# Optimization experiments

Measured on AMD Instinct MI355X. Metric: run time of the kernel, lower is better.

The kernel has to match this reference:

```python
import jax, jax.numpy as jnp
import numpy as np

TEMPERATURE = 32.0  # sqrt(d_model=1024)

def setup_inputs() -> dict:
    key = jax.random.key(0)
    kq, kk, kv = jax.random.split(key, 3)
    B, H, S, D = 2, 16, 2048, 64
    q = jax.random.normal(kq, (B, H, S, D), dtype=jnp.float32)
    k = jax.random.normal(kk, (B, H, S, D), dtype=jnp.float32)
    v = jax.random.normal(kv, (B, H, S, D), dtype=jnp.float32)
    mask = jnp.ones((B, 1, 1, S), dtype=jnp.int32)  # key-padding mask, 1 = keep
    return {"q": q, "k": k, "v": v, "mask": mask}

def reference(q, k, v, mask):
    # scores: [B,H,S,S]
    scores = jnp.einsum('bhqd,bhkd->bhqk', q / TEMPERATURE, k)
    scores = jnp.where(mask == 0, jnp.float32(-1e9), scores)
    attention = jax.nn.softmax(scores, axis=-1)
    # dropout is identity at inference (module's nn.Dropout in eval mode)
    output = jnp.einsum('bhqk,bhkd->bhqd', attention, v)
    return (output, attention)
```

## Files before the change

kernel.cpp:

```cpp
#include <hip/hip_runtime.h>
#include <hip/hip_bf16.h>


#define S_LEN 2048
#define D_DIM 64
#define BM 64
#define BN 64
#define NT (S_LEN / BN)
#define LDP 72

typedef __attribute__((ext_vector_type(8))) short bf16x8;
typedef __attribute__((ext_vector_type(4))) float f32x4;

__device__ __forceinline__ unsigned short f2bf(float x) {
    unsigned u = __float_as_uint(x);
    u += 0x7FFF + ((u >> 16) & 1);
    return (unsigned short)(u >> 16);
}

__global__ __launch_bounds__(256, 4)
void attn_kernel(const float* __restrict__ Qg, const float* __restrict__ Kg,
                 const float* __restrict__ Vg, const int* __restrict__ Mg,
                 float* __restrict__ Og, float* __restrict__ Ag) {
    __shared__ unsigned short Qs[BM * LDP];
    __shared__ unsigned short Ks[BN * LDP];
    __shared__ unsigned short Vts[D_DIM * LDP];
    __shared__ unsigned short Ps[BM * LDP];
    __shared__ int maskS[BN];

    const int tid  = threadIdx.x;
    const int w    = tid >> 6;
    const int lane = tid & 63;
    const int l15  = lane & 15;
    const int quad = lane >> 4;

    const int qt = blockIdx.x;
    const int bh = blockIdx.y;
    const int b  = bh >> 4;
    const int q0 = qt * BM;

    const float* Qb = Qg + ((size_t)bh * S_LEN + q0) * D_DIM;
    const float* Kb = Kg + (size_t)bh * S_LEN * D_DIM;
    const float* Vb = Vg + (size_t)bh * S_LEN * D_DIM;
    const int*   Mb = Mg + (size_t)b * S_LEN;
    float* Ob = Og + ((size_t)bh * S_LEN + q0) * D_DIM;
    float* Ab = Ag + ((size_t)bh * S_LEN + q0) * (size_t)S_LEN;

    {
        const float sc = 1.0f / 32.0f;
        #pragma unroll
        for (int i = 0; i < 4; ++i) {
            int f = tid + i * 256;
            int row = f >> 4, c4 = f & 15;
            const float4 v = *(const float4*)(Qb + row * D_DIM + c4 * 4);
            unsigned lo = f2bf(v.x * sc) | ((unsigned)f2bf(v.y * sc) << 16);
            unsigned hi = f2bf(v.z * sc) | ((unsigned)f2bf(v.w * sc) << 16);
            *(uint2*)(&Qs[row * LDP + c4 * 4]) = make_uint2(lo, hi);
        }
    }
    __syncthreads();

    bf16x8 aq[2];
    #pragma unroll
    for (int ks = 0; ks < 2; ++ks)
        aq[ks] = *(const bf16x8*)(&Qs[(w * 16 + l15) * LDP + ks * 32 + quad * 8]);

    float lsum[4] = {0.f, 0.f, 0.f, 0.f};

    for (int kt = 0; kt < NT; ++kt) {
        const int key0 = kt * BN;
        #pragma unroll
        for (int i = 0; i < 4; ++i) {
            int f = tid + i * 256;
            int row = f >> 4, c4 = f & 15;
            const float4 v = *(const float4*)(Kb + (size_t)(key0 + row) * D_DIM + c4 * 4);
            unsigned lo = f2bf(v.x) | ((unsigned)f2bf(v.y) << 16);
            unsigned hi = f2bf(v.z) | ((unsigned)f2bf(v.w) << 16);
            *(uint2*)(&Ks[row * LDP + c4 * 4]) = make_uint2(lo, hi);
        }
        if (tid < BN) maskS[tid] = Mb[key0 + tid];
        __syncthreads();

        #pragma unroll
        for (int cb = 0; cb < 4; ++cb) {
            f32x4 acc = {0.f, 0.f, 0.f, 0.f};
            #pragma unroll
            for (int ks = 0; ks < 2; ++ks) {
                bf16x8 bk = *(const bf16x8*)(&Ks[(cb * 16 + l15) * LDP + ks * 32 + quad * 8]);
                acc = __builtin_amdgcn_mfma_f32_16x16x32_bf16(aq[ks], bk, acc, 0, 0, 0);
            }
            const int mk = maskS[cb * 16 + l15];
            #pragma unroll
            for (int r = 0; r < 4; ++r) {
                float s = mk ? acc[r] : -1e9f;
                lsum[r] += __expf(s);
            }
        }
        __syncthreads();
    }

    #pragma unroll
    for (int r = 0; r < 4; ++r) {
        float v = lsum[r];
        v += __shfl_xor(v, 1);
        v += __shfl_xor(v, 2);
        v += __shfl_xor(v, 4);
        v += __shfl_xor(v, 8);
        lsum[r] = 1.0f / v;
    }

    f32x4 oacc[4];
    #pragma unroll
    for (int db = 0; db < 4; ++db) oacc[db] = (f32x4){0.f, 0.f, 0.f, 0.f};

    for (int kt = 0; kt < NT; ++kt) {
        const int key0 = kt * BN;
        #pragma unroll
        for (int i = 0; i < 4; ++i) {
            int f = tid + i * 256;
            int row = f >> 4, c4 = f & 15;
            const float4 v = *(const float4*)(Kb + (size_t)(key0 + row) * D_DIM + c4 * 4);
            unsigned lo = f2bf(v.x) | ((unsigned)f2bf(v.y) << 16);
            unsigned hi = f2bf(v.z) | ((unsigned)f2bf(v.w) << 16);
            *(uint2*)(&Ks[row * LDP + c4 * 4]) = make_uint2(lo, hi);
        }
        {
            int key = tid & 63, g = tid >> 6;
            #pragma unroll
            for (int i = 0; i < 4; ++i) {
                int d0 = (g * 4 + i) * 4;
                const float4 v = *(const float4*)(Vb + (size_t)(key0 + key) * D_DIM + d0);
                Vts[(d0 + 0) * LDP + key] = f2bf(v.x);
                Vts[(d0 + 1) * LDP + key] = f2bf(v.y);
                Vts[(d0 + 2) * LDP + key] = f2bf(v.z);
                Vts[(d0 + 3) * LDP + key] = f2bf(v.w);
            }
        }
        if (tid < BN) maskS[tid] = Mb[key0 + tid];
        __syncthreads();

        #pragma unroll
        for (int cb = 0; cb < 4; ++cb) {
            f32x4 acc = {0.f, 0.f, 0.f, 0.f};
            #pragma unroll
            for (int ks = 0; ks < 2; ++ks) {
                bf16x8 bk = *(const bf16x8*)(&Ks[(cb * 16 + l15) * LDP + ks * 32 + quad * 8]);
                acc = __builtin_amdgcn_mfma_f32_16x16x32_bf16(aq[ks], bk, acc, 0, 0, 0);
            }
            const int mk  = maskS[cb * 16 + l15];
            const int key = key0 + cb * 16 + l15;
            #pragma unroll
            for (int r = 0; r < 4; ++r) {
                float s = mk ? acc[r] : -1e9f;
                float p = __expf(s) * lsum[r];
                int row = w * 16 + quad * 4 + r;
                Ab[(size_t)row * S_LEN + key] = p;
                Ps[row * LDP + cb * 16 + l15] = f2bf(p);
            }
        }
        #pragma unroll
        for (int ks2 = 0; ks2 < 2; ++ks2) {
            bf16x8 ap = *(const bf16x8*)(&Ps[(w * 16 + l15) * LDP + ks2 * 32 + quad * 8]);
            #pragma unroll
            for (int db = 0; db < 4; ++db) {
                bf16x8 bv = *(const bf16x8*)(&Vts[(db * 16 + l15) * LDP + ks2 * 32 + quad * 8]);
                oacc[db] = __builtin_amdgcn_mfma_f32_16x16x32_bf16(ap, bv, oacc[db], 0, 0, 0);
            }
        }
        __syncthreads();
    }

    #pragma unroll
    for (int db = 0; db < 4; ++db) {
        #pragma unroll
        for (int r = 0; r < 4; ++r) {
            int row = w * 16 + quad * 4 + r;
            Ob[(size_t)row * D_DIM + db * 16 + l15] = oacc[db][r];
        }
    }
}

extern "C" void kernel_launch(void* const* d_in, const int* in_sizes, int n_in,
                              void* d_out, int out_size, void* d_ws, size_t ws_size,
                              hipStream_t stream) {
    const float* q = (const float*)d_in[0];
    const float* k = (const float*)d_in[1];
    const float* v = (const float*)d_in[2];
    const int* mask = (const int*)d_in[3];
    float* out = (float*)d_out;
    float* attn = out + (size_t)2 * 16 * 2048 * 64;

    dim3 grid(S_LEN / BM, 2 * 16);
    dim3 block(256);
    attn_kernel<<<grid, block, 0, stream>>>(q, k, v, mask, out, attn);
}
```

Before: 767.8 us.

## Pre-convert K and transposed V to bf16 in workspace, vectorize attention stores

Adds two pre-pass kernels that convert K to bf16 and V to transposed bf16 in workspace, so the attention kernel copies ready bf16 tiles instead of re-converting fp32 K and V in every query block. It also folds log2(e) into the Q scale so exp2 can be used, swaps the MFMA operand order so each lane holds four contiguous keys, and writes the attention and output with 16-byte nontemporal stores. A fallback path is kept when no workspace is available. The cost is two extra launches and extra workspace traffic.

After: 704.5 us. -8.2%, faster.

```diff
diff --git a/kernel.cpp b/kernel.cpp
--- a/kernel.cpp
+++ b/kernel.cpp
@@ -8,24 +8,63 @@
 #define BN 64
 #define NT (S_LEN / BN)
 #define LDP 72
+#define BH_N 32
 
 typedef __attribute__((ext_vector_type(8))) short bf16x8;
 typedef __attribute__((ext_vector_type(4))) float f32x4;
 
-__device__ __forceinline__ unsigned short f2bf(float x) {
-    unsigned u = __float_as_uint(x);
-    u += 0x7FFF + ((u >> 16) & 1);
-    return (unsigned short)(u >> 16);
-}
-
+__device__ __forceinline__ unsigned pack_bf16(float a, float b) {
+    union { __hip_bfloat162 h; unsigned u; } cv;
+    cv.h = __float22bfloat162_rn(make_float2(a, b));
+    return cv.u;
+}
+__device__ __forceinline__ unsigned short bf1(float x) {
+    union { __hip_bfloat16 h; unsigned short u; } cv;
+    cv.h = __float2bfloat16(x);
+    return cv.u;
+}
+
+__global__ __launch_bounds__(256)
+void conv_k(const float* __restrict__ Kg, unsigned short* __restrict__ Kw) {
+    size_t i = (size_t)(blockIdx.x * 256 + threadIdx.x) * 8;
+    const float4 v0 = *(const float4*)(Kg + i);
+    const float4 v1 = *(const float4*)(Kg + i + 4);
+    uint4 o;
+    o.x = pack_bf16(v0.x, v0.y);
+    o.y = pack_bf16(v0.z, v0.w);
+    o.z = pack_bf16(v1.x, v1.y);
+    o.w = pack_bf16(v1.z, v1.w);
+    *(uint4*)(Kw + i) = o;
+}
+
+__global__ __launch_bounds__(256)
+void conv_vt(const float* __restrict__ Vg, unsigned short* __restrict__ Vtw) {
+    const int bh = blockIdx.y;
+    const int d  = threadIdx.x & 63;
+    const int kq = threadIdx.x >> 6;
+    const int key0 = blockIdx.x * 32 + kq * 8;
+    const float* Vb = Vg + ((size_t)bh * S_LEN + key0) * D_DIM + d;
+    float f[8];
+    #pragma unroll
+    for (int i = 0; i < 8; ++i) f[i] = Vb[i * D_DIM];
+    uint4 o;
+    o.x = pack_bf16(f[0], f[1]);
+    o.y = pack_bf16(f[2], f[3]);
+    o.z = pack_bf16(f[4], f[5]);
+    o.w = pack_bf16(f[6], f[7]);
+    *(uint4*)(Vtw + ((size_t)bh * D_DIM + d) * S_LEN + key0) = o;
+}
+
+template <int PRE>
 __global__ __launch_bounds__(256, 4)
 void attn_kernel(const float* __restrict__ Qg, const float* __restrict__ Kg,
                  const float* __restrict__ Vg, const int* __restrict__ Mg,
+                 const unsigned short* __restrict__ Kw,
+                 const unsigned short* __restrict__ Vtw,
                  float* __restrict__ Og, float* __restrict__ Ag) {
-    __shared__ unsigned short Qs[BM * LDP];
     __shared__ unsigned short Ks[BN * LDP];
-    __shared__ unsigned short Vts[D_DIM * LDP];
     __shared__ unsigned short Ps[BM * LDP];
+    __shared__ unsigned short QV[D_DIM * LDP];
     __shared__ int maskS[BN];
 
     const int tid  = threadIdx.x;
@@ -38,24 +77,22 @@
     const int bh = blockIdx.y;
     const int b  = bh >> 4;
     const int q0 = qt * BM;
+    const int qrow = w * 16 + l15;
 
     const float* Qb = Qg + ((size_t)bh * S_LEN + q0) * D_DIM;
-    const float* Kb = Kg + (size_t)bh * S_LEN * D_DIM;
-    const float* Vb = Vg + (size_t)bh * S_LEN * D_DIM;
     const int*   Mb = Mg + (size_t)b * S_LEN;
     float* Ob = Og + ((size_t)bh * S_LEN + q0) * D_DIM;
     float* Ab = Ag + ((size_t)bh * S_LEN + q0) * (size_t)S_LEN;
 
     {
-        const float sc = 1.0f / 32.0f;
+        const float sc = 0.04508422f;
         #pragma unroll
         for (int i = 0; i < 4; ++i) {
             int f = tid + i * 256;
             int row = f >> 4, c4 = f & 15;
             const float4 v = *(const float4*)(Qb + row * D_DIM + c4 * 4);
-            unsigned lo = f2bf(v.x * sc) | ((unsigned)f2bf(v.y * sc) << 16);
-            unsigned hi = f2bf(v.z * sc) | ((unsigned)f2bf(v.w * sc) << 16);
-            *(uint2*)(&Qs[row * LDP + c4 * 4]) = make_uint2(lo, hi);
+            *(uint2*)(&QV[row * LDP + c4 * 4]) =
+                make_uint2(pack_bf16(v.x * sc, v.y * sc), pack_bf16(v.z * sc, v.w * sc));
         }
     }
     __syncthreads();
@@ -63,21 +100,36 @@
     bf16x8 aq[2];
     #pragma unroll
     for (int ks = 0; ks < 2; ++ks)
-        aq[ks] = *(const bf16x8*)(&Qs[(w * 16 + l15) * LDP + ks * 32 + quad * 8]);
-
-    float lsum[4] = {0.f, 0.f, 0.f, 0.f};
+        aq[ks] = *(const bf16x8*)(&QV[qrow * LDP + ks * 32 + quad * 8]);
+
+    auto stage_k = [&](int key0) {
+        if constexpr (PRE) {
+            const unsigned short* Kt = Kw + (size_t)bh * S_LEN * D_DIM + (size_t)key0 * D_DIM;
+            #pragma unroll
+            for (int i = 0; i < 2; ++i) {
+                int idx = tid + i * 256;
+                int row = idx >> 3, c = idx & 7;
+                uint4 vv = *(const uint4*)(Kt + row * D_DIM + c * 8);
+                *(uint4*)(&Ks[row * LDP + c * 8]) = vv;
+            }
+        } else {
+            const float* Kb = Kg + ((size_t)bh * S_LEN + key0) * D_DIM;
+            #pragma unroll
+            for (int i = 0; i < 4; ++i) {
+                int f = tid + i * 256;
+                int row = f >> 4, c4 = f & 15;
+                const float4 v = *(const float4*)(Kb + row * D_DIM + c4 * 4);
+                *(uint2*)(&Ks[row * LDP + c4 * 4]) =
+                    make_uint2(pack_bf16(v.x, v.y), pack_bf16(v.z, v.w));
+            }
+        }
+    };
+
+    float lsum = 0.f;
 
     for (int kt = 0; kt < NT; ++kt) {
         const int key0 = kt * BN;
-        #pragma unroll
-        for (int i = 0; i < 4; ++i) {
-            int f = tid + i * 256;
-            int row = f >> 4, c4 = f & 15;
-            const float4 v = *(const float4*)(Kb + (size_t)(key0 + row) * D_DIM + c4 * 4);
-            unsigned lo = f2bf(v.x) | ((unsigned)f2bf(v.y) << 16);
-            unsigned hi = f2bf(v.z) | ((unsigned)f2bf(v.w) << 16);
-            *(uint2*)(&Ks[row * LDP + c4 * 4]) = make_uint2(lo, hi);
-        }
+        stage_k(key0);
         if (tid < BN) maskS[tid] = Mb[key0 + tid];
         __syncthreads();
 
@@ -87,27 +139,21 @@
             #pragma unroll
             for (int ks = 0; ks < 2; ++ks) {
                 bf16x8 bk = *(const bf16x8*)(&Ks[(cb * 16 + l15) * LDP + ks * 32 + quad * 8]);
-                acc = __builtin_amdgcn_mfma_f32_16x16x32_bf16(aq[ks], bk, acc, 0, 0, 0);
-            }
-            const int mk = maskS[cb * 16 + l15];
-            #pragma unroll
-            for (int r = 0; r < 4; ++r) {
-                float s = mk ? acc[r] : -1e9f;
-                lsum[r] += __expf(s);
-            }
-        }
-        __syncthreads();
-    }
-
-    #pragma unroll
-    for (int r = 0; r < 4; ++r) {
-        float v = lsum[r];
-        v += __shfl_xor(v, 1);
-        v += __shfl_xor(v, 2);
-        v += __shfl_xor(v, 4);
-        v += __shfl_xor(v, 8);
-        lsum[r] = 1.0f / v;
-    }
+                acc = __builtin_amdgcn_mfma_f32_16x16x32_bf16(bk, aq[ks], acc, 0, 0, 0);
+            }
+            const int4 m4 = *(const int4*)(&maskS[cb * 16 + quad * 4]);
+            float e0 = m4.x ? __builtin_exp2f(acc[0]) : 0.f;
+            float e1 = m4.y ? __builtin_exp2f(acc[1]) : 0.f;
+            float e2 = m4.z ? __builtin_exp2f(acc[2]) : 0.f;
+            float e3 = m4.w ? __builtin_exp2f(acc[3]) : 0.f;
+            lsum += (e0 + e1) + (e2 + e3);
+        }
+        __syncthreads();
+    }
+
+    lsum += __shfl_xor(lsum, 16);
+    lsum += __shfl_xor(lsum, 32);
+    const float linv = 1.0f / lsum;
 
     f32x4 oacc[4];
     #pragma unroll
@@ -115,25 +161,26 @@
 
     for (int kt = 0; kt < NT; ++kt) {
         const int key0 = kt * BN;
-        #pragma unroll
-        for (int i = 0; i < 4; ++i) {
-            int f = tid + i * 256;
-            int row = f >> 4, c4 = f & 15;
-            const float4 v = *(const float4*)(Kb + (size_t)(key0 + row) * D_DIM + c4 * 4);
-            unsigned lo = f2bf(v.x) | ((unsigned)f2bf(v.y) << 16);
-            unsigned hi = f2bf(v.z) | ((unsigned)f2bf(v.w) << 16);
-            *(uint2*)(&Ks[row * LDP + c4 * 4]) = make_uint2(lo, hi);
-        }
-        {
+        stage_k(key0);
+        if constexpr (PRE) {
+            const unsigned short* Vt = Vtw + (size_t)bh * D_DIM * S_LEN + key0;
+            #pragma unroll
+            for (int i = 0; i < 2; ++i) {
+                int idx = tid + i * 256;
+                int d = idx >> 3, c = idx & 7;
+                uint4 vv = *(const uint4*)(Vt + (size_t)d * S_LEN + c * 8);
+                *(uint4*)(&QV[d * LDP + c * 8]) = vv;
+            }
+        } else {
             int key = tid & 63, g = tid >> 6;
             #pragma unroll
             for (int i = 0; i < 4; ++i) {
                 int d0 = (g * 4 + i) * 4;
-                const float4 v = *(const float4*)(Vb + (size_t)(key0 + key) * D_DIM + d0);
-                Vts[(d0 + 0) * LDP + key] = f2bf(v.x);
-                Vts[(d0 + 1) * LDP + key] = f2bf(v.y);
-                Vts[(d0 + 2) * LDP + key] = f2bf(v.z);
-                Vts[(d0 + 3) * LDP + key] = f2bf(v.w);
+                const float4 v = *(const float4*)(Vg + ((size_t)bh * S_LEN + key0 + key) * D_DIM + d0);
+                QV[(d0 + 0) * LDP + key] = bf1(v.x);
+                QV[(d0 + 1) * LDP + key] = bf1(v.y);
+                QV[(d0 + 2) * LDP + key] = bf1(v.z);
+                QV[(d0 + 3) * LDP + key] = bf1(v.w);
             }
         }
         if (tid < BN) maskS[tid] = Mb[key0 + tid];
@@ -145,26 +192,27 @@
             #pragma unroll
             for (int ks = 0; ks < 2; ++ks) {
                 bf16x8 bk = *(const bf16x8*)(&Ks[(cb * 16 + l15) * LDP + ks * 32 + quad * 8]);
-                acc = __builtin_amdgcn_mfma_f32_16x16x32_bf16(aq[ks], bk, acc, 0, 0, 0);
-            }
-            const int mk  = maskS[cb * 16 + l15];
-            const int key = key0 + cb * 16 + l15;
-            #pragma unroll
-            for (int r = 0; r < 4; ++r) {
-                float s = mk ? acc[r] : -1e9f;
-                float p = __expf(s) * lsum[r];
-                int row = w * 16 + quad * 4 + r;
-                Ab[(size_t)row * S_LEN + key] = p;
-                Ps[row * LDP + cb * 16 + l15] = f2bf(p);
-            }
-        }
+                acc = __builtin_amdgcn_mfma_f32_16x16x32_bf16(bk, aq[ks], acc, 0, 0, 0);
+            }
+            const int4 m4 = *(const int4*)(&maskS[cb * 16 + quad * 4]);
+            f32x4 p;
+            p[0] = (m4.x ? __builtin_exp2f(acc[0]) : 0.f) * linv;
+            p[1] = (m4.y ? __builtin_exp2f(acc[1]) : 0.f) * linv;
+            p[2] = (m4.z ? __builtin_exp2f(acc[2]) : 0.f) * linv;
+            p[3] = (m4.w ? __builtin_exp2f(acc[3]) : 0.f) * linv;
+            __builtin_nontemporal_store(
+                p, (f32x4*)(Ab + (size_t)qrow * S_LEN + key0 + cb * 16 + quad * 4));
+            *(uint2*)(&Ps[qrow * LDP + cb * 16 + quad * 4]) =
+                make_uint2(pack_bf16(p[0], p[1]), pack_bf16(p[2], p[3]));
+        }
+
         #pragma unroll
         for (int ks2 = 0; ks2 < 2; ++ks2) {
-            bf16x8 ap = *(const bf16x8*)(&Ps[(w * 16 + l15) * LDP + ks2 * 32 + quad * 8]);
+            bf16x8 ap = *(const bf16x8*)(&Ps[qrow * LDP + ks2 * 32 + quad * 8]);
             #pragma unroll
             for (int db = 0; db < 4; ++db) {
-                bf16x8 bv = *(const bf16x8*)(&Vts[(db * 16 + l15) * LDP + ks2 * 32 + quad * 8]);
-                oacc[db] = __builtin_amdgcn_mfma_f32_16x16x32_bf16(ap, bv, oacc[db], 0, 0, 0);
+                bf16x8 bv = *(const bf16x8*)(&QV[(db * 16 + l15) * LDP + ks2 * 32 + quad * 8]);
+                oacc[db] = __builtin_amdgcn_mfma_f32_16x16x32_bf16(bv, ap, oacc[db], 0, 0, 0);
             }
         }
         __syncthreads();
@@ -172,11 +220,9 @@
 
     #pragma unroll
     for (int db = 0; db < 4; ++db) {
-        #pragma unroll
-        for (int r = 0; r < 4; ++r) {
-            int row = w * 16 + quad * 4 + r;
-            Ob[(size_t)row * D_DIM + db * 16 + l15] = oacc[db][r];
-        }
+        f32x4 o4 = oacc[db];
+        __builtin_nontemporal_store(
+            o4, (f32x4*)(Ob + (size_t)qrow * D_DIM + db * 16 + quad * 4));
     }
 }
 
@@ -190,7 +236,18 @@
     float* out = (float*)d_out;
     float* attn = out + (size_t)2 * 16 * 2048 * 64;
 
-    dim3 grid(S_LEN / BM, 2 * 16);
+    const size_t kw_elems = (size_t)BH_N * S_LEN * D_DIM;
+    const size_t need = 2 * kw_elems * sizeof(unsigned short);
     dim3 block(256);
-    attn_kernel<<<grid, block, 0, stream>>>(q, k, v, mask, out, attn);
-}
+    dim3 grid(S_LEN / BM, BH_N);
+
+    if (d_ws && ws_size >= need) {
+        unsigned short* Kw  = (unsigned short*)d_ws;
+        unsigned short* Vtw = Kw + kw_elems;
+        conv_k<<<dim3((unsigned)(kw_elems / 8 / 256)), block, 0, stream>>>(k, Kw);
+        conv_vt<<<dim3(S_LEN / 32, BH_N), block, 0, stream>>>(v, Vtw);
+        attn_kernel<1><<<grid, block, 0, stream>>>(q, k, v, mask, Kw, Vtw, out, attn);
+    } else {
+        attn_kernel<0><<<grid, block, 0, stream>>>(q, k, v, mask, nullptr, nullptr, out, attn);
+    }
+}
```
